# Kernel tuning notes

Measured on AMD Instinct MI355X. Metric: run time of the kernel, lower is better.

The kernel has to match this reference:

```python
import jax, jax.numpy as jnp
import numpy as np

HEADS = 16


def bemm(x, weight, bias, er, es):
    # BatchEnsembleMM.forward: x [T,B,Hin], weight [Hout,Hin], er [B,Hin], es [B,Hout]
    x_r = x * er[None, :, :]
    x_mm = jnp.einsum('tbh,oh->tbo', x_r, weight)
    return x_mm * es[None, :, :] + bias


def rel_shift(x):
    # RelativeShift.forward (batch_first): x [N, len_q, len_r]
    n, q, r = x.shape
    x_pad = jnp.pad(x, ((0, 0), (0, 0), (1, 0)))        # [N, q, r+1]
    x_view = x_pad.reshape(n, r + 1, q)[:, 1:, :]        # drop first 'row'
    return x_view.reshape(n, q, r)


def setup_inputs() -> dict:
    key = jax.random.key(0)
    ks = jax.random.split(key, 14)
    T, B, H = 1024, 8, 1024
    Lr = 1024
    s = 0.02
    return {
        'inputs': jax.random.normal(ks[0], (T, B, H), jnp.float32),
        'pos': jax.random.normal(ks[1], (Lr, 1, H), jnp.float32),
        'input_weights': jax.random.normal(ks[2], (3 * H, H), jnp.float32) * s,
        'input_biases': jax.random.normal(ks[3], (3 * H,), jnp.float32) * s,
        'pos_weights': jax.random.normal(ks[4], (H, H), jnp.float32) * s,
        'pos_biases': jax.random.normal(ks[5], (H,), jnp.float32) * s,
        'output_weights': jax.random.normal(ks[6], (H, H), jnp.float32) * s,
        'output_biases': jax.random.normal(ks[7], (H,), jnp.float32) * s,
        'r_i': 1.0 + jax.random.normal(ks[8], (B, H), jnp.float32) * 0.1,
        's_i': 1.0 + jax.random.normal(ks[9], (B, 3 * H), jnp.float32) * 0.1,
        'r_p': 1.0 + jax.random.normal(ks[10], (B, H), jnp.float32) * 0.1,
        's_p': 1.0 + jax.random.normal(ks[11], (B, H), jnp.float32) * 0.1,
        'r_w_bias': jax.random.normal(ks[12], (HEADS, H // HEADS), jnp.float32) * s,
        'r_r_bias': jax.random.normal(ks[13], (HEADS, H // HEADS), jnp.float32) * s,
        'heads': HEADS,
    }


def reference(inputs, pos, input_weights, input_biases, pos_weights, pos_biases,
              output_weights, output_biases, r_i, s_i, r_p, s_p,
              r_w_bias, r_r_bias, heads):
    T, B, H = inputs.shape
    hd = H // heads
    scale = hd ** (-0.5)
    Lr = pos.shape[0]

    pos_rep = jnp.broadcast_to(pos, (Lr, B, H))

    # BatchEnsemble QKV and positional projections (training path)
    qkv = bemm(inputs, input_weights, input_biases, r_i, s_i)       # [T,B,3H]
    qkv = qkv.reshape(T, B * heads, 3, hd)
    queries, keys, values = qkv[:, :, 0, :], qkv[:, :, 1, :], qkv[:, :, 2, :]

    r_head_k = bemm(pos_rep, pos_weights, pos_biases, r_p, s_p)     # [Lr,B,H]
    r_head_k = r_head_k.reshape(Lr, B * heads, hd)

    rw_head_q = (queries.reshape(T, B, heads, hd) + r_w_bias).reshape(T, B * heads, hd)
    rr_head_q = (queries.reshape(T, B, heads, hd) + r_r_bias).reshape(T, B * heads, hd)

    # content score AC and position score BD
    matmul_ac = jnp.einsum('qnd,knd->nqk', rw_head_q, keys) * scale    # [B*h,T,T]
    matmul_bd = jnp.einsum('qnd,rnd->nqr', rr_head_q, r_head_k) * scale
    matmul_bd = rel_shift(matmul_bd)[:, :, :T]

    attn_score = matmul_ac + matmul_bd
    softmax_results = jax.nn.softmax(attn_score.astype(jnp.float32), axis=-1).astype(inputs.dtype)

    context = jnp.einsum('nqk,knd->qnd', softmax_results, values).reshape(T, B, H)
    outputs = jnp.einsum('tbh,oh->tbo', context, output_weights) + output_biases
    return outputs
```

## Files before the change

kernel.cpp:

```cpp
#include <hip/hip_runtime.h>
#include <cstdint>
#include <cstddef>

using u16 = unsigned short;
typedef short short8 __attribute__((ext_vector_type(8)));
typedef unsigned short us8 __attribute__((ext_vector_type(8)));
typedef unsigned short us4 __attribute__((ext_vector_type(4)));
typedef float f32x4 __attribute__((ext_vector_type(4)));
typedef float f4 __attribute__((ext_vector_type(4)));

#define T_ 1024
#define B_ 8
#define H_ 1024
#define HEADS_ 16
#define HD_ 64
#define N3_ 3072

__device__ __forceinline__ float b2f(u16 u){
  union { float f; unsigned int i; } v; v.i = ((unsigned int)u) << 16; return v.f;
}
__device__ __forceinline__ u16 f2b(float f){
  union { float f; unsigned int i; } v; v.f = f;
  return (u16)((v.i + 0x8000u) >> 16);
}

template<bool HAS_S, bool SCALE_A, bool POS_A, bool A_BF16, bool OUT_F32>
__global__ __launch_bounds__(256) void k_gemm(const void* __restrict__ A_, const float* __restrict__ W,
                                              const float* __restrict__ RA, const float* __restrict__ S,
                                              const float* __restrict__ bias, void* __restrict__ C_, int N){
  const int K = 1024;
  const int n0 = blockIdx.x * 128, m0 = blockIdx.y * 128;
  const int tid = threadIdx.x, lane = tid & 63;
  const int wave = tid >> 6, wr = wave >> 1, wc = wave & 1;
  __shared__ alignas(16) u16 At[128 * 32];
  __shared__ alignas(16) u16 Bt[128 * 32];
  f32x4 acc[4][4] = {};

  for (int kt = 0; kt < 32; ++kt){
    const int k0 = kt * 32;
    f4 wv[4];
    us8 avb[2];
    f4 avf[4];
#pragma unroll
    for (int i = 0; i < 4; ++i){
      int c = tid + i * 256, r = c >> 3, sg = c & 7;
      wv[i] = *(const f4*)(W + (size_t)(n0 + r) * K + k0 + sg * 4);
    }
    if (A_BF16){
      const u16* A = (const u16*)A_;
#pragma unroll
      for (int i = 0; i < 2; ++i){
        int c = tid + i * 256, r = c >> 2, sg = c & 3;
        avb[i] = *(const us8*)(A + (size_t)(m0 + r) * K + k0 + sg * 8);
      }
    } else {
      const float* A = (const float*)A_;
#pragma unroll
      for (int i = 0; i < 4; ++i){
        int c = tid + i * 256, r = c >> 3, sg = c & 7;
        int m = m0 + r;
        const float* ap = POS_A ? (A + (size_t)(m >> 3) * K + k0 + sg * 4)
                                : (A + (size_t)m * K + k0 + sg * 4);
        avf[i] = *(const f4*)ap;
        if (SCALE_A){
          f4 rv = *(const f4*)(RA + (m & 7) * K + k0 + sg * 4);
          avf[i] = avf[i] * rv;
        }
      }
    }
    __syncthreads();
#pragma unroll
    for (int i = 0; i < 4; ++i){
      int c = tid + i * 256, r = c >> 3, sg = c & 7;
      us4 pw;
#pragma unroll
      for (int u = 0; u < 4; ++u) pw[u] = f2b(wv[i][u]);
      *(us4*)(Bt + r * 32 + sg * 4) = pw;
    }
    if (A_BF16){
#pragma unroll
      for (int i = 0; i < 2; ++i){
        int c = tid + i * 256, r = c >> 2, sg = c & 3;
        *(us8*)(At + r * 32 + sg * 8) = avb[i];
      }
    } else {
#pragma unroll
      for (int i = 0; i < 4; ++i){
        int c = tid + i * 256, r = c >> 3, sg = c & 7;
        us4 pa;
#pragma unroll
        for (int u = 0; u < 4; ++u) pa[u] = f2b(avf[i][u]);
        *(us4*)(At + r * 32 + sg * 4) = pa;
      }
    }
    __syncthreads();
    short8 af[4], bf[4];
#pragma unroll
    for (int i = 0; i < 4; ++i){
      int ar = wr * 64 + i * 16 + (lane & 15);
      af[i] = *(const short8*)(At + ar * 32 + ((lane >> 4) << 3));
      int br = wc * 64 + i * 16 + (lane & 15);
      bf[i] = *(const short8*)(Bt + br * 32 + ((lane >> 4) << 3));
    }
#pragma unroll
    for (int i = 0; i < 4; ++i)
#pragma unroll
      for (int j = 0; j < 4; ++j)
        acc[i][j] = __builtin_amdgcn_mfma_f32_16x16x32_bf16(af[i], bf[j], acc[i][j], 0, 0, 0);
  }
#pragma unroll
  for (int i = 0; i < 4; ++i){
    int row0 = wr * 64 + i * 16 + ((lane >> 4) << 2);
#pragma unroll
    for (int j = 0; j < 4; ++j){
      int o = n0 + wc * 64 + j * 16 + (lane & 15);
      float bv = bias[o];
#pragma unroll
      for (int jj = 0; jj < 4; ++jj){
        int m = m0 + row0 + jj;
        float v = acc[i][j][jj];
        if (HAS_S) v *= S[(m & 7) * N + o];
        v += bv;
        if (OUT_F32) ((float*)C_)[(size_t)m * N + o] = v;
        else         ((u16*)C_)[(size_t)m * N + o] = f2b(v);
      }
    }
  }
}

__global__ __launch_bounds__(256) void k_vt(const u16* __restrict__ qkv, u16* __restrict__ VT){
  const int tt = blockIdx.x;
  const int n = blockIdx.y;
  const int b = n >> 4, head = n & 15;
  __shared__ alignas(16) u16 tile[64][72];
  const int tid = threadIdx.x;
#pragma unroll
  for (int i = 0; i < 2; ++i){
    int c = tid + i * 256;
    int r = c >> 3, sg = c & 7;
    const u16* src = qkv + ((size_t)(tt * 64 + r) * 8 + b) * N3_ + head * 192 + 128 + sg * 8;
    *(us8*)&tile[r][sg * 8] = *(const us8*)src;
  }
  __syncthreads();
#pragma unroll
  for (int i = 0; i < 2; ++i){
    int c = tid + i * 256;
    int d = c >> 3, sg = c & 7;
    us8 ov;
#pragma unroll
    for (int u = 0; u < 8; ++u) ov[u] = tile[sg * 8 + u][d];
    *(us8*)(VT + ((size_t)n * 64 + d) * 1024 + tt * 64 + sg * 8) = ov;
  }
}

#define G_OFF   0
#define KV_OFF  67856
#define RWQ_OFF 133392
#define RRQ_OFF 137488
#define RED_OFF 143632
#define SMEM_SZ 145808

__device__ __forceinline__ int gswz(int byt){ return byt ^ (((byt >> 13) & 3) << 5); }

__global__ __launch_bounds__(512, 1) void k_attn(const u16* __restrict__ qkv, const u16* __restrict__ rk,
                                                 const u16* __restrict__ VTg, const float* __restrict__ rwb,
                                                 const float* __restrict__ rrb, u16* __restrict__ ctx){
  const int n = blockIdx.x, qb = blockIdx.y, q0 = qb * 32;
  const int bat = n >> 4, head = n & 15;
  const int tid = threadIdx.x, lane = tid & 63, wave = tid >> 6;
  const int l15 = lane & 15, grp = lane >> 4;

  __shared__ alignas(16) char smem[SMEM_SZ];
  char* gB  = smem + G_OFF;
  char* kvS = smem + KV_OFF;
  u16* rwq = (u16*)(smem + RWQ_OFF);
  u16* rrq = (u16*)(smem + RRQ_OFF);
  float* redf = (float*)(smem + RED_OFF);

#pragma unroll
  for (int rep = 0; rep < 2; ++rep){
    int c = tid + rep * 512;
    if (c < 640){
      int s = c >> 3, sg = c & 7;
      u16* dst; int row; const float* bias;
      if (s < 32){ dst = rwq; row = s; bias = rwb; }
      else       { dst = rrq; row = s - 32; bias = rrb; }
      int qrow = q0 + row;
      float v[8];
      const float* bp2 = bias + head * 64 + sg * 8;
      if (qrow < T_){
        const u16* qp = qkv + ((size_t)qrow * 8 + bat) * N3_ + head * 192 + sg * 8;
        us8 qv = *(const us8*)qp;
        f4 b0 = *(const f4*)bp2, b1 = *(const f4*)(bp2 + 4);
#pragma unroll
        for (int u = 0; u < 4; ++u){
          v[u]     = (b2f(qv[u])     + b0[u]) * 0.125f;
          v[u + 4] = (b2f(qv[u + 4]) + b1[u]) * 0.125f;
        }
      } else {
#pragma unroll
        for (int u = 0; u < 8; ++u) v[u] = 0.f;
      }
      us8 pk;
#pragma unroll
      for (int u = 0; u < 8; ++u) pk[u] = f2b(v[u]);
      *(us8*)((char*)dst + row * 128 + ((sg * 16) ^ ((row & 7) << 4))) = pk;
    }
  }
  if (tid < 33) *(u16*)(gB + gswz(tid * 2050 + 2048)) = 0;

  auto ldf = [&](const void* base, int row, int kkb)->short8 {
    int co = kkb + (grp << 4);
    return *(const short8*)((const char*)base + row * 128 + (co ^ ((row & 7) << 4)));
  };

  us8 stv[8];

#pragma unroll
  for (int i = 0; i < 8; ++i){ int c = tid + i * 512, r = c >> 3, sg = c & 7;
    stv[i] = *(const us8*)(rk + ((size_t)r * 8 + bat) * 1024 + head * 64 + sg * 8); }
  __syncthreads();
#pragma unroll
  for (int i = 0; i < 8; ++i){ int c = tid + i * 512, r = c >> 3, sg = c & 7;
    *(us8*)(kvS + r * 128 + ((sg * 16) ^ ((r & 7) << 4))) = stv[i]; }
#pragma unroll
  for (int i = 0; i < 8; ++i){ int c = tid + i * 512, r = c >> 3, sg = c & 7;
    stv[i] = *(const us8*)(rk + ((size_t)(512 + r) * 8 + bat) * 1024 + head * 64 + sg * 8); }
  __syncthreads();

#pragma unroll
  for (int s = 0; s < 2; ++s){
    short8 af[3][2];
#pragma unroll
    for (int pi = 0; pi < 3; ++pi)
#pragma unroll
      for (int kk = 0; kk < 2; ++kk) af[pi][kk] = ldf(rrq, pi * 16 + l15, kk * 64);
#pragma unroll
    for (int c4 = 0; c4 < 4; ++c4){
      int brow = wave * 64 + c4 * 16 + l15;
      short8 bf0 = ldf(kvS, brow, 0), bf1 = ldf(kvS, brow, 64);
      int rg = s * 512 + wave * 64 + c4 * 16 + l15;
#pragma unroll
      for (int pi = 0; pi < 3; ++pi){
        f32x4 acc = {0.f, 0.f, 0.f, 0.f};
        acc = __builtin_amdgcn_mfma_f32_16x16x32_bf16(af[pi][0], bf0, acc, 0, 0, 0);
        acc = __builtin_amdgcn_mfma_f32_16x16x32_bf16(af[pi][1], bf1, acc, 0, 0, 0);
#pragma unroll
        for (int jj = 0; jj < 4; ++jj){
          int a = pi * 16 + (grp << 2) + jj;
          if (a < 33) *(u16*)(gB + gswz(a * 2050 + (rg << 1))) = f2b(acc[jj]);
        }
      }
    }
    if (s == 0){
      __syncthreads();
#pragma unroll
      for (int i = 0; i < 8; ++i){ int c = tid + i * 512, r = c >> 3, sg = c & 7;
        *(us8*)(kvS + r * 128 + ((sg * 16) ^ ((r & 7) << 4))) = stv[i]; }
      __syncthreads();
    }
  }

  f32x4 p[2][2][4];
  float pm[2][4];
#pragma unroll
  for (int m = 0; m < 2; ++m)
#pragma unroll
    for (int jj = 0; jj < 4; ++jj) pm[m][jj] = -3.0e38f;

#pragma unroll
  for (int i = 0; i < 8; ++i){ int c = tid + i * 512, r = c >> 3, sg = c & 7;
    stv[i] = *(const us8*)(qkv + ((size_t)r * 8 + bat) * N3_ + head * 192 + 64 + sg * 8); }
  __syncthreads();
#pragma unroll
  for (int i = 0; i < 8; ++i){ int c = tid + i * 512, r = c >> 3, sg = c & 7;
    *(us8*)(kvS + r * 128 + ((sg * 16) ^ ((r & 7) << 4))) = stv[i]; }
#pragma unroll
  for (int i = 0; i < 8; ++i){ int c = tid + i * 512, r = c >> 3, sg = c & 7;
    stv[i] = *(const us8*)(qkv + ((size_t)(512 + r) * 8 + bat) * N3_ + head * 192 + 64 + sg * 8); }
  __syncthreads();

#pragma unroll
  for (int s = 0; s < 2; ++s){
    short8 af[2][2];
#pragma unroll
    for (int m = 0; m < 2; ++m)
#pragma unroll
      for (int kk = 0; kk < 2; ++kk) af[m][kk] = ldf(rwq, m * 16 + l15, kk * 64);
#pragma unroll
    for (int c4 = 0; c4 < 4; ++c4){
      int brow = wave * 64 + c4 * 16 + l15;
      short8 bf0 = ldf(kvS, brow, 0), bf1 = ldf(kvS, brow, 64);
      int bcol = s * 512 + wave * 64 + c4 * 16 + l15;
      int byt0 = ((1023 - q0 + bcol) << 1) + (grp << 13);
#pragma unroll
      for (int m = 0; m < 2; ++m){
        f32x4 acc = {0.f, 0.f, 0.f, 0.f};
        acc = __builtin_amdgcn_mfma_f32_16x16x32_bf16(af[m][0], bf0, acc, 0, 0, 0);
        acc = __builtin_amdgcn_mfma_f32_16x16x32_bf16(af[m][1], bf1, acc, 0, 0, 0);
#pragma unroll
        for (int jj = 0; jj < 4; ++jj){
          int byt = byt0 + (m << 15) + (jj << 11);
          float gv = b2f(*(const u16*)(gB + gswz(byt)));
          float sc = acc[jj] + gv;
          p[s][m][c4][jj] = sc;
          pm[m][jj] = fmaxf(pm[m][jj], sc);
        }
      }
    }
    if (s == 0){
      __syncthreads();
#pragma unroll
      for (int i = 0; i < 8; ++i){ int c = tid + i * 512, r = c >> 3, sg = c & 7;
        *(us8*)(kvS + r * 128 + ((sg * 16) ^ ((r & 7) << 4))) = stv[i]; }
      __syncthreads();
    }
  }

#pragma unroll
  for (int m = 0; m < 2; ++m)
#pragma unroll
    for (int jj = 0; jj < 4; ++jj)
#pragma unroll
      for (int mk = 1; mk < 16; mk <<= 1) pm[m][jj] = fmaxf(pm[m][jj], __shfl_xor(pm[m][jj], mk));
  __syncthreads();
  if (l15 == 0){
#pragma unroll
    for (int m = 0; m < 2; ++m)
#pragma unroll
      for (int jj = 0; jj < 4; ++jj) redf[wave * 32 + m * 16 + (grp << 2) + jj] = pm[m][jj];
  }
  __syncthreads();
  float M_[2][4];
#pragma unroll
  for (int m = 0; m < 2; ++m)
#pragma unroll
    for (int jj = 0; jj < 4; ++jj){
      int row = m * 16 + (grp << 2) + jj;
      float v = redf[row];
#pragma unroll
      for (int w = 1; w < 8; ++w) v = fmaxf(v, redf[w * 32 + row]);
      M_[m][jj] = v;
    }
  float L_[2][4] = {};
#pragma unroll
  for (int s = 0; s < 2; ++s)
#pragma unroll
    for (int m = 0; m < 2; ++m)
#pragma unroll
      for (int c4 = 0; c4 < 4; ++c4)
#pragma unroll
        for (int jj = 0; jj < 4; ++jj){
          float e = __expf(fminf(p[s][m][c4][jj] - M_[m][jj], 0.f));
          p[s][m][c4][jj] = e;
          L_[m][jj] += e;
        }
#pragma unroll
  for (int m = 0; m < 2; ++m)
#pragma unroll
    for (int jj = 0; jj < 4; ++jj)
#pragma unroll
      for (int mk = 1; mk < 16; mk <<= 1) L_[m][jj] += __shfl_xor(L_[m][jj], mk);
  if (l15 == 0){
#pragma unroll
    for (int m = 0; m < 2; ++m)
#pragma unroll
      for (int jj = 0; jj < 4; ++jj) redf[256 + wave * 32 + m * 16 + (grp << 2) + jj] = L_[m][jj];
  }
  __syncthreads();
  if (wave == 0 && l15 == 0){
#pragma unroll
    for (int m = 0; m < 2; ++m)
#pragma unroll
      for (int jj = 0; jj < 4; ++jj){
        int row = m * 16 + (grp << 2) + jj;
        float sum = 0.f;
#pragma unroll
        for (int w = 0; w < 8; ++w) sum += redf[256 + w * 32 + row];
        redf[512 + row] = 1.0f / (sum + 1e-20f);
      }
  }

  char* ptW = smem + G_OFF + wave * 8192;
#pragma unroll
  for (int s = 0; s < 2; ++s)
#pragma unroll
    for (int m = 0; m < 2; ++m)
#pragma unroll
      for (int c4 = 0; c4 < 4; ++c4)
#pragma unroll
        for (int jj = 0; jj < 4; ++jj){
          int q = m * 16 + (grp << 2) + jj;
          int tl = s * 64 + c4 * 16 + l15;
          *(u16*)(ptW + q * 256 + ((tl * 2) ^ ((q & 7) << 4))) = f2b(p[s][m][c4][jj]);
        }
#pragma unroll
  for (int i = 0; i < 8; ++i){ int c = tid + i * 512, d = c >> 6, tc = c & 63;
    stv[i] = *(const us8*)(VTg + ((size_t)n * 64 + d) * 1024 + tc * 8); }
  __syncthreads();
#pragma unroll
  for (int i = 0; i < 8; ++i){ int c = tid + i * 512, d = c >> 6, tc = c & 63;
    *(us8*)(kvS + d * 1024 + ((tc * 16) ^ ((d & 31) << 4))) = stv[i]; }
#pragma unroll
  for (int i = 0; i < 8; ++i){ int c = tid + i * 512, d = c >> 6, tc = c & 63;
    stv[i] = *(const us8*)(VTg + ((size_t)n * 64 + d) * 1024 + 512 + tc * 8); }
  __syncthreads();

  f32x4 Oacc[2][4] = {};
#pragma unroll
  for (int s = 0; s < 2; ++s){
#pragma unroll
    for (int kk = 0; kk < 2; ++kk){
      short8 pa[2];
#pragma unroll
      for (int m = 0; m < 2; ++m)
        pa[m] = *(const short8*)(ptW + (m * 16 + l15) * 256 + ((s * 128 + kk * 64 + (grp << 4)) ^ ((l15 & 7) << 4)));
#pragma unroll
      for (int dt = 0; dt < 4; ++dt){
        int dr = dt * 16 + l15;
        short8 vb = *(const short8*)(kvS + dr * 1024 + ((wave * 128 + kk * 64 + (grp << 4)) ^ ((dr & 31) << 4)));
#pragma unroll
        for (int m = 0; m < 2; ++m)
          Oacc[m][dt] = __builtin_amdgcn_mfma_f32_16x16x32_bf16(pa[m], vb, Oacc[m][dt], 0, 0, 0);
      }
    }
    if (s == 0){
      __syncthreads();
#pragma unroll
      for (int i = 0; i < 8; ++i){ int c = tid + i * 512, d = c >> 6, tc = c & 63;
        *(us8*)(kvS + d * 1024 + ((tc * 16) ^ ((d & 31) << 4))) = stv[i]; }
      __syncthreads();
    }
  }

  __syncthreads();
  float* par = (float*)kvS;
#pragma unroll
  for (int m = 0; m < 2; ++m)
#pragma unroll
    for (int dt = 0; dt < 4; ++dt)
#pragma unroll
      for (int jj = 0; jj < 4; ++jj)
        par[wave * 2048 + (m * 16 + (grp << 2) + jj) * 64 + dt * 16 + l15] = Oacc[m][dt][jj];
  __syncthreads();
  {
    f32x4 v = {0.f, 0.f, 0.f, 0.f};
#pragma unroll
    for (int w = 0; w < 8; ++w) v += *(const f32x4*)(par + w * 2048 + tid * 4);
    int q = tid >> 4, d4 = (tid & 15) * 4;
    float il = redf[512 + q];
    us4 pk;
#pragma unroll
    for (int e = 0; e < 4; ++e) pk[e] = f2b(v[e] * il);
    *(us4*)(ctx + ((size_t)(q0 + q) * 8 + bat) * 1024 + head * 64 + d4) = pk;
  }
}

extern "C" void kernel_launch(void* const* d_in, const int* in_sizes, int n_in,
                              void* d_out, int out_size, void* d_ws, size_t ws_size,
                              hipStream_t stream){
  const float* x   = (const float*)d_in[0];
  const float* pos = (const float*)d_in[1];
  const float* Wi  = (const float*)d_in[2];
  const float* bi  = (const float*)d_in[3];
  const float* Wp  = (const float*)d_in[4];
  const float* bp  = (const float*)d_in[5];
  const float* Wo  = (const float*)d_in[6];
  const float* bo  = (const float*)d_in[7];
  const float* r_i = (const float*)d_in[8];
  const float* s_i = (const float*)d_in[9];
  const float* r_p = (const float*)d_in[10];
  const float* s_p = (const float*)d_in[11];
  const float* rwb = (const float*)d_in[12];
  const float* rrb = (const float*)d_in[13];

  const size_t MB = 1024 * 1024;
  u16* qkv = (u16*)((char*)d_ws);
  u16* rk  = (u16*)((char*)d_ws + 48 * MB);
  u16* VTg  = (u16*)d_out;
  u16* ctxg = (u16*)((char*)d_out + 16777216);

  k_gemm<true,  true,  false, false, false><<<dim3(24, 64), 256, 0, stream>>>(x,   Wi, r_i, s_i, bi, qkv, N3_);
  k_gemm<true,  true,  true,  false, false><<<dim3(8, 64),  256, 0, stream>>>(pos, Wp, r_p, s_p, bp, rk, 1024);
  k_vt<<<dim3(16, 128), 256, 0, stream>>>(qkv, VTg);
  k_attn<<<dim3(128, 32), 512, 0, stream>>>(qkv, rk, VTg, rwb, rrb, ctxg);
  hipMemcpyAsync(qkv, ctxg, (size_t)out_size * sizeof(u16), hipMemcpyDeviceToDevice, stream);
  k_gemm<false, false, false, true, true><<<dim3(8, 64), 256, 0, stream>>>(qkv, Wo, nullptr, nullptr, bo, (float*)d_out, 1024);
}
```

Before: 451.6 us.

## Prefetch next K/V tiles across phases, remap block order, use exp2 softmax

```diff
diff --git a/kernel.cpp b/kernel.cpp
--- a/kernel.cpp
+++ b/kernel.cpp
@@ -165,7 +165,10 @@
 __global__ __launch_bounds__(512, 1) void k_attn(const u16* __restrict__ qkv, const u16* __restrict__ rk,
                                                  const u16* __restrict__ VTg, const float* __restrict__ rwb,
                                                  const float* __restrict__ rrb, u16* __restrict__ ctx){
-  const int n = blockIdx.x, qb = blockIdx.y, q0 = qb * 32;
+  const int bid = blockIdx.x;
+  const int n = (bid & 7) + ((bid >> 8) << 3);
+  const int qb = (bid >> 3) & 31;
+  const int q0 = qb * 32;
   const int bat = n >> 4, head = n & 15;
   const int tid = threadIdx.x, lane = tid & 63, wave = tid >> 6;
   const int l15 = lane & 15, grp = lane >> 4;
@@ -177,6 +180,13 @@
   u16* rrq = (u16*)(smem + RRQ_OFF);
   float* redf = (float*)(smem + RED_OFF);
 
+  us8 stv[8];
+
+#pragma unroll
+  for (int i = 0; i < 8; ++i){ int c = tid + i * 512, r = c >> 3, sg = c & 7;
+    stv[i] = *(const us8*)(rk + ((size_t)r * 8 + bat) * 1024 + head * 64 + sg * 8); }
+
+  const float PRESCALE = 0.125f * 1.44269504089f;
 #pragma unroll
   for (int rep = 0; rep < 2; ++rep){
     int c = tid + rep * 512;
@@ -194,8 +204,8 @@
         f4 b0 = *(const f4*)bp2, b1 = *(const f4*)(bp2 + 4);
 #pragma unroll
         for (int u = 0; u < 4; ++u){
-          v[u]     = (b2f(qv[u])     + b0[u]) * 0.125f;
-          v[u + 4] = (b2f(qv[u + 4]) + b1[u]) * 0.125f;
+          v[u]     = (b2f(qv[u])     + b0[u]) * PRESCALE;
+          v[u + 4] = (b2f(qv[u + 4]) + b1[u]) * PRESCALE;
         }
       } else {
 #pragma unroll
@@ -213,23 +223,12 @@
     int co = kkb + (grp << 4);
     return *(const short8*)((const char*)base + row * 128 + (co ^ ((row & 7) << 4)));
   };
-
-  us8 stv[8];
-
-#pragma unroll
-  for (int i = 0; i < 8; ++i){ int c = tid + i * 512, r = c >> 3, sg = c & 7;
-    stv[i] = *(const us8*)(rk + ((size_t)r * 8 + bat) * 1024 + head * 64 + sg * 8); }
-  __syncthreads();
-#pragma unroll
-  for (int i = 0; i < 8; ++i){ int c = tid + i * 512, r = c >> 3, sg = c & 7;
-    *(us8*)(kvS + r * 128 + ((sg * 16) ^ ((r & 7) << 4))) = stv[i]; }
-#pragma unroll
-  for (int i = 0; i < 8; ++i){ int c = tid + i * 512, r = c >> 3, sg = c & 7;
-    stv[i] = *(const us8*)(rk + ((size_t)(512 + r) * 8 + bat) * 1024 + head * 64 + sg * 8); }
-  __syncthreads();
-
-#pragma unroll
-  for (int s = 0; s < 2; ++s){
+  auto stageKV = [&](){
+#pragma unroll
+    for (int i = 0; i < 8; ++i){ int c = tid + i * 512, r = c >> 3, sg = c & 7;
+      *(us8*)(kvS + r * 128 + ((sg * 16) ^ ((r & 7) << 4))) = stv[i]; }
+  };
+  auto computeB = [&](int s){
     short8 af[3][2];
 #pragma unroll
     for (int pi = 0; pi < 3; ++pi)
@@ -252,14 +251,22 @@
         }
       }
     }
-    if (s == 0){
-      __syncthreads();
-#pragma unroll
-      for (int i = 0; i < 8; ++i){ int c = tid + i * 512, r = c >> 3, sg = c & 7;
-        *(us8*)(kvS + r * 128 + ((sg * 16) ^ ((r & 7) << 4))) = stv[i]; }
-      __syncthreads();
-    }
-  }
+  };
+
+  __syncthreads();
+  stageKV();
+#pragma unroll
+  for (int i = 0; i < 8; ++i){ int c = tid + i * 512, r = c >> 3, sg = c & 7;
+    stv[i] = *(const us8*)(rk + ((size_t)(512 + r) * 8 + bat) * 1024 + head * 64 + sg * 8); }
+  __syncthreads();
+  computeB(0);
+  __syncthreads();
+  stageKV();
+#pragma unroll
+  for (int i = 0; i < 8; ++i){ int c = tid + i * 512, r = c >> 3, sg = c & 7;
+    stv[i] = *(const us8*)(qkv + ((size_t)r * 8 + bat) * N3_ + head * 192 + 64 + sg * 8); }
+  __syncthreads();
+  computeB(1);
 
   f32x4 p[2][2][4];
   float pm[2][4];
@@ -268,20 +275,7 @@
 #pragma unroll
     for (int jj = 0; jj < 4; ++jj) pm[m][jj] = -3.0e38f;
 
-#pragma unroll
-  for (int i = 0; i < 8; ++i){ int c = tid + i * 512, r = c >> 3, sg = c & 7;
-    stv[i] = *(const us8*)(qkv + ((size_t)r * 8 + bat) * N3_ + head * 192 + 64 + sg * 8); }
-  __syncthreads();
-#pragma unroll
-  for (int i = 0; i < 8; ++i){ int c = tid + i * 512, r = c >> 3, sg = c & 7;
-    *(us8*)(kvS + r * 128 + ((sg * 16) ^ ((r & 7) << 4))) = stv[i]; }
-#pragma unroll
-  for (int i = 0; i < 8; ++i){ int c = tid + i * 512, r = c >> 3, sg = c & 7;
-    stv[i] = *(const us8*)(qkv + ((size_t)(512 + r) * 8 + bat) * N3_ + head * 192 + 64 + sg * 8); }
-  __syncthreads();
-
-#pragma unroll
-  for (int s = 0; s < 2; ++s){
+  auto computeC = [&](int s){
     short8 af[2][2];
 #pragma unroll
     for (int m = 0; m < 2; ++m)
@@ -308,14 +302,19 @@
         }
       }
     }
-    if (s == 0){
-      __syncthreads();
-#pragma unroll
-      for (int i = 0; i < 8; ++i){ int c = tid + i * 512, r = c >> 3, sg = c & 7;
-        *(us8*)(kvS + r * 128 + ((sg * 16) ^ ((r & 7) << 4))) = stv[i]; }
-      __syncthreads();
-    }
-  }
+  };
+
+  __syncthreads();
+  stageKV();
+#pragma unroll
+  for (int i = 0; i < 8; ++i){ int c = tid + i * 512, r = c >> 3, sg = c & 7;
+    stv[i] = *(const us8*)(qkv + ((size_t)(512 + r) * 8 + bat) * N3_ + head * 192 + 64 + sg * 8); }
+  __syncthreads();
+  computeC(0);
+  __syncthreads();
+  stageKV();
+  __syncthreads();
+  computeC(1);
 
 #pragma unroll
   for (int m = 0; m < 2; ++m)
@@ -324,6 +323,9 @@
 #pragma unroll
       for (int mk = 1; mk < 16; mk <<= 1) pm[m][jj] = fmaxf(pm[m][jj], __shfl_xor(pm[m][jj], mk));
   __syncthreads();
+#pragma unroll
+  for (int i = 0; i < 8; ++i){ int c = tid + i * 512, d = c >> 6, tc = c & 63;
+    stv[i] = *(const us8*)(VTg + ((size_t)n * 64 + d) * 1024 + tc * 8); }
   if (l15 == 0){
 #pragma unroll
     for (int m = 0; m < 2; ++m)
@@ -342,6 +344,13 @@
       for (int w = 1; w < 8; ++w) v = fmaxf(v, redf[w * 32 + row]);
       M_[m][jj] = v;
     }
+#pragma unroll
+  for (int i = 0; i < 8; ++i){ int c = tid + i * 512, d = c >> 6, tc = c & 63;
+    *(us8*)(kvS + d * 1024 + ((tc * 16) ^ ((d & 31) << 4))) = stv[i]; }
+#pragma unroll
+  for (int i = 0; i < 8; ++i){ int c = tid + i * 512, d = c >> 6, tc = c & 63;
+    stv[i] = *(const us8*)(VTg + ((size_t)n * 64 + d) * 1024 + 512 + tc * 8); }
+
   float L_[2][4] = {};
 #pragma unroll
   for (int s = 0; s < 2; ++s)
@@ -351,7 +360,7 @@
       for (int c4 = 0; c4 < 4; ++c4)
 #pragma unroll
         for (int jj = 0; jj < 4; ++jj){
-          float e = __expf(fminf(p[s][m][c4][jj] - M_[m][jj], 0.f));
+          float e = __builtin_exp2f(p[s][m][c4][jj] - M_[m][jj]);
           p[s][m][c4][jj] = e;
           L_[m][jj] += e;
         }
@@ -394,16 +403,6 @@
           int tl = s * 64 + c4 * 16 + l15;
           *(u16*)(ptW + q * 256 + ((tl * 2) ^ ((q & 7) << 4))) = f2b(p[s][m][c4][jj]);
         }
-#pragma unroll
-  for (int i = 0; i < 8; ++i){ int c = tid + i * 512, d = c >> 6, tc = c & 63;
-    stv[i] = *(const us8*)(VTg + ((size_t)n * 64 + d) * 1024 + tc * 8); }
-  __syncthreads();
-#pragma unroll
-  for (int i = 0; i < 8; ++i){ int c = tid + i * 512, d = c >> 6, tc = c & 63;
-    *(us8*)(kvS + d * 1024 + ((tc * 16) ^ ((d & 31) << 4))) = stv[i]; }
-#pragma unroll
-  for (int i = 0; i < 8; ++i){ int c = tid + i * 512, d = c >> 6, tc = c & 63;
-    stv[i] = *(const us8*)(VTg + ((size_t)n * 64 + d) * 1024 + 512 + tc * 8); }
   __syncthreads();
 
   f32x4 Oacc[2][4] = {};
@@ -483,7 +482,7 @@
   k_gemm<true,  true,  false, false, false><<<dim3(24, 64), 256, 0, stream>>>(x,   Wi, r_i, s_i, bi, qkv, N3_);
   k_gemm<true,  true,  true,  false, false><<<dim3(8, 64),  256, 0, stream>>>(pos, Wp, r_p, s_p, bp, rk, 1024);
   k_vt<<<dim3(16, 128), 256, 0, stream>>>(qkv, VTg);
-  k_attn<<<dim3(128, 32), 512, 0, stream>>>(qkv, rk, VTg, rwb, rrb, ctxg);
+  k_attn<<<dim3(4096), 512, 0, stream>>>(qkv, rk, VTg, rwb, rrb, ctxg);
   hipMemcpyAsync(qkv, ctxg, (size_t)out_size * sizeof(u16), hipMemcpyDeviceToDevice, stream);
   k_gemm<false, false, false, true, true><<<dim3(8, 64), 256, 0, stream>>>(qkv, Wo, nullptr, nullptr, bo, (float*)d_out, 1024);
 }
```

After: 455.2 us. No clear change (+0.8%).
